# Optimization experiments

Measured on AMD Instinct MI355X. Metric: run time of the kernel, lower is better.

The kernel has to match this reference:

```python
import jax, jax.numpy as jnp
import numpy as np

WS, WS2, UP = 8, 16, 2
DIM, HEADS = 192, 6
HD = DIM // HEADS
SCALE = HD ** -0.5
EPS = 1e-5

def _rel_index():
    r1, c1 = np.meshgrid(np.arange(WS), np.arange(WS), indexing='ij')
    r2, c2 = np.meshgrid(np.arange(WS2), np.arange(WS2), indexing='ij')
    r1, c1 = r1.ravel(), c1.ravel()          # 64 query positions
    r2, c2 = r2.ravel(), c2.ravel()          # 256 kv positions
    rel_row = r1[:, None] - r2[None, :]
    rel_col = c1[:, None] - c2[None, :]
    off = WS * UP - 1    # 15
    span = WS + WS * UP - 1  # 23
    return jnp.asarray((rel_row + off) * span + (rel_col + off))  # (64, 256)

REL_IDX = _rel_index()

def layer_norm(x, w, b):
    m = x.mean(-1, keepdims=True)
    v = ((x - m) ** 2).mean(-1, keepdims=True)
    return (x - m) * jax.lax.rsqrt(v + EPS) * w + b

def window_partition(x, ws):
    B, H, W, C = x.shape
    x = x.reshape(B, H // ws, ws, W // ws, ws, C).transpose(0, 1, 3, 2, 4, 5)
    return x.reshape(-1, ws * ws, C)

def window_reverse(w, ws, H, W, B):
    x = w.reshape(B, H // ws, W // ws, ws, ws, -1).transpose(0, 1, 3, 2, 4, 5)
    return x.reshape(B, H, W, -1)

def setup_inputs() -> dict:
    key = jax.random.key(0)
    ks = jax.random.split(key, 8)
    B, H, W, H2, W2 = 4, 128, 128, 256, 256
    s = 0.02
    return {
        'x': jax.random.normal(ks[0], (B, H * W, DIM), jnp.float32),
        'x2': jax.random.normal(ks[1], (B, H2 * W2, DIM), jnp.float32),
        'norm1_w': jnp.ones((DIM,), jnp.float32),
        'norm1_b': jnp.zeros((DIM,), jnp.float32),
        'qkv_w': jax.random.normal(ks[2], (DIM, DIM), jnp.float32) * s,
        'qkv_b': jnp.zeros((DIM,), jnp.float32),
        'qkv2_w': jax.random.normal(ks[3], (2 * DIM, DIM), jnp.float32) * s,
        'qkv2_b': jnp.zeros((2 * DIM,), jnp.float32),
        'rel_bias': jax.random.normal(ks[4], (23 * 23, HEADS), jnp.float32) * s,
        'proj_w': jax.random.normal(ks[5], (DIM, DIM), jnp.float32) * s,
        'proj_b': jnp.zeros((DIM,), jnp.float32),
        'norm2_w': jnp.ones((DIM,), jnp.float32),
        'norm2_b': jnp.zeros((DIM,), jnp.float32),
        'fc1_w': jax.random.normal(ks[6], (4 * DIM, DIM), jnp.float32) * s,
        'fc1_b': jnp.zeros((4 * DIM,), jnp.float32),
        'fc2_w': jax.random.normal(ks[7], (DIM, 4 * DIM), jnp.float32) * s,
        'fc2_b': jnp.zeros((DIM,), jnp.float32),
        'H': 128, 'W': 128, 'H2': 256, 'W2': 256,
    }

def reference(x, x2, norm1_w, norm1_b, qkv_w, qkv_b, qkv2_w, qkv2_b, rel_bias,
              proj_w, proj_b, norm2_w, norm2_b, fc1_w, fc1_b, fc2_w, fc2_b,
              H, W, H2, W2):
    B, L, C = x.shape
    shortcut = x
    xn = layer_norm(x, norm1_w, norm1_b).reshape(B, H, W, C)
    x2r = x2.reshape(B, H2, W2, C)

    xw = window_partition(xn, WS)      # (nW, 64, C)
    x2w = window_partition(x2r, WS2)   # (nW, 256, C)

    q = (xw @ qkv_w.T + qkv_b).reshape(-1, WS * WS, HEADS, HD).transpose(0, 2, 1, 3)
    kv = (x2w @ qkv2_w.T + qkv2_b).reshape(-1, WS2 * WS2, 2, HEADS, HD).transpose(2, 0, 3, 1, 4)
    k, v = kv[0], kv[1]                # (nW, h, 256, d)

    attn = jnp.einsum('whnd,whmd->whnm', q * SCALE, k)   # (nW, h, 64, 256)
    bias = rel_bias[REL_IDX]                             # (64, 256, h)
    attn = attn + bias.transpose(2, 0, 1)[None]
    attn = jax.nn.softmax(attn, axis=-1)
    out = jnp.einsum('whnm,whmd->wnhd', attn, v).reshape(-1, WS * WS, C)
    out = out @ proj_w.T + proj_b

    x = shortcut + window_reverse(out, WS, H, W, B).reshape(B, H * W, C)
    h = layer_norm(x, norm2_w, norm2_b)
    h = jax.nn.gelu(h @ fc1_w.T + fc1_b, approximate=False)
    x = x + (h @ fc2_w.T + fc2_b)
    return x
```

## Files before the change

### kernel.cpp

```cpp
#include <hip/hip_runtime.h>
#include <hip/hip_bf16.h>
#include <math.h>

typedef unsigned int u32;
typedef unsigned short u16;

typedef __attribute__((ext_vector_type(8))) short bf16x8;
typedef __attribute__((ext_vector_type(4))) float f32x4;

__device__ __forceinline__ float bflo(u32 u){ union{u32 i; float f;} c; c.i = u << 16; return c.f; }
__device__ __forceinline__ float bfhi(u32 u){ union{u32 i; float f;} c; c.i = u & 0xffff0000u; return c.f; }
__device__ __forceinline__ float bfs(u16 s){ union{u32 i; float f;} c; c.i = ((u32)s) << 16; return c.f; }
__device__ __forceinline__ u32 packbf(float a, float b){
  union{float f; u32 i;} ca, cb; ca.f = a; cb.f = b;
  u32 ua = (ca.i + 0x7fffu + ((ca.i >> 16) & 1u)) >> 16;
  u32 ub = (cb.i + 0x7fffu + ((cb.i >> 16) & 1u)) >> 16;
  return (ua & 0xffffu) | (ub << 16);
}
__device__ __forceinline__ u16 bf1(float a){
  union{float f; u32 i;} c; c.f = a;
  return (u16)((c.i + 0x7fffu + ((c.i >> 16) & 1u)) >> 16);
}
__device__ __forceinline__ bf16x8 pack8(float f0,float f1,float f2,float f3,
                                        float f4,float f5,float f6,float f7){
  union { u32 u[4]; bf16x8 v; } cv;
  cv.u[0]=packbf(f0,f1); cv.u[1]=packbf(f2,f3); cv.u[2]=packbf(f4,f5); cv.u[3]=packbf(f6,f7);
  return cv.v;
}
__device__ __forceinline__ float gelu_exact(float v){ return 0.5f*v*(1.0f + erff(v*0.70710678118654752f)); }
__device__ __forceinline__ bool detect_f32(const u32* rawn1){ return (rawn1[0] & 0xFFFFu) == 0u; }

#define SCALE_Q 0.17677669529663687f

#define P_N1W 0
#define P_N1B 192
#define P_N2W 384
#define P_N2B 576
#define P_QKVB 768
#define P_QKV2B 960
#define P_PROJB 1344
#define P_FC1B 1536
#define P_FC2B 2304
#define P_RELB 2496
#define P_TOTAL 5670
#define W_QKV 0
#define W_QKV2 18432
#define W_PROJ 55296
#define W_FC1 73728
#define W_FC2 147456
#define W_TOTAL 221184

__device__ __forceinline__ void stage_w64x192(const u32* __restrict__ src, u32* lds, int tid){
  #pragma unroll
  for (int t = 0; t < 6; ++t) {
    int idx = tid + t*256;
    int j = idx / 24, seg = idx % 24;
    uint4 v = *(const uint4*)(src + (size_t)j*96 + seg*4);
    int byt = (j*384 + seg*16) ^ ((j&7)<<4);
    *(uint4*)((char*)lds + byt) = v;
  }
}
__device__ __forceinline__ bf16x8 lds_w64(const u32* lds, int j, int kt, int g){
  int byt = (j*384 + kt*64 + g*16) ^ ((j&7)<<4);
  return *(const bf16x8*)((const char*)lds + byt);
}
__device__ __forceinline__ bf16x8 lds_w192(const u32* lds, int j, int kk, int g){
  int byt = (j*128 + kk*64 + g*16) ^ ((j&7)<<4);
  return *(const bf16x8*)((const char*)lds + byt);
}

typedef __attribute__((address_space(1))) const u32 gas_u32c;
typedef __attribute__((address_space(3))) u32 las_u32;
__device__ __forceinline__ void gld_lds16(const u32* g, u32* l){
  gas_u32c* gp = (gas_u32c*)(unsigned long long)(size_t)g;
  las_u32*  lp = (las_u32*)(unsigned int)(size_t)l;
  __builtin_amdgcn_global_load_lds(gp, lp, 16, 0, 0);
}
__device__ __forceinline__ void issue_w64x192(const u32* src, u32* lds, int w, int l){
  #pragma unroll
  for (int t = 0; t < 3; ++t) {
    int seg = w + t*8;
    int a = seg*1024 + l*16;
    int j = a / 384;
    int off = a - j*384;
    const u32* g = src + (size_t)j*96 + ((off ^ ((j&7)<<4)) >> 2);
    gld_lds16(g, lds + seg*256);
  }
}
__device__ __forceinline__ void issue_w192x64(const u32* src, int ch, u32* lds, int w, int l){
  #pragma unroll
  for (int t = 0; t < 3; ++t) {
    int seg = w + t*8;
    int a = seg*1024 + l*16;
    int j = a >> 7;
    int off = a & 127;
    const u32* g = src + (size_t)j*384 + ch*32 + ((off ^ ((j&7)<<4)) >> 2);
    gld_lds16(g, lds + seg*256);
  }
}

__global__ __launch_bounds__(256) void k_canon_w(
    const void* qkvw, const void* qkv2w, const void* projw,
    const void* fc1w, const void* fc2w, const u32* rawn1, u32* cw)
{
  int idx = blockIdx.x*256 + threadIdx.x;
  bool isf32 = detect_f32(rawn1);
  const void* src; int off;
  if      (idx < W_QKV2){ src=qkvw;  off=idx; }
  else if (idx < W_PROJ){ src=qkv2w; off=idx-W_QKV2; }
  else if (idx < W_FC1) { src=projw; off=idx-W_PROJ; }
  else if (idx < W_FC2) { src=fc1w;  off=idx-W_FC1; }
  else                  { src=fc2w;  off=idx-W_FC2; }
  u32 o;
  if (isf32) { float2 v = ((const float2*)src)[off]; o = packbf(v.x, v.y); }
  else       { o = ((const u32*)src)[off]; }
  cw[idx] = o;
}

__global__ __launch_bounds__(256) void k_canon_v(
    const void* n1w, const void* n1b, const void* n2w, const void* n2b,
    const void* qkvb, const void* qkv2b, const void* projb,
    const void* fc1b, const void* fc2b, const void* relb,
    const u32* rawn1, float* par)
{
  int idx = blockIdx.x*256 + threadIdx.x;
  if (idx >= P_TOTAL) return;
  bool isf32 = detect_f32(rawn1);
  const void* src; int off;
  if      (idx < P_N1B)  { src=n1w;  off=idx; }
  else if (idx < P_N2W)  { src=n1b;  off=idx-P_N1B; }
  else if (idx < P_N2B)  { src=n2w;  off=idx-P_N2W; }
  else if (idx < P_QKVB) { src=n2b;  off=idx-P_N2B; }
  else if (idx < P_QKV2B){ src=qkvb; off=idx-P_QKVB; }
  else if (idx < P_PROJB){ src=qkv2b;off=idx-P_QKV2B; }
  else if (idx < P_FC1B) { src=projb;off=idx-P_PROJB; }
  else if (idx < P_FC2B) { src=fc1b; off=idx-P_FC1B; }
  else if (idx < P_RELB) { src=fc2b; off=idx-P_FC2B; }
  else                   { src=relb; off=idx-P_RELB; }
  par[idx] = isf32 ? ((const float*)src)[off] : bfs(((const u16*)src)[off]);
}

__global__ __launch_bounds__(256) void k_bias(
    const float* __restrict__ par, float* __restrict__ tbl)
{
  int idx = blockIdx.x*256 + threadIdx.x;
  int h  = idx >> 12;
  int remi = idx & 4095;
  int kt = remi >> 8;
  int qt = (remi >> 6) & 3;
  int ll = idx & 63;
  int lr = ll & 15, g = ll >> 4;
  int q = qt*16 + lr;
  int r1 = q >> 3, c1 = q & 7;
  float vv[4];
  #pragma unroll
  for (int i = 0; i < 4; ++i) {
    int kv = kt*16 + 4*g + i;
    int r2 = kv >> 4, c2 = kv & 15;
    vv[i] = par[P_RELB + ((r1-r2+15)*23 + (c1-c2+15))*6 + h];
  }
  ((float4*)tbl)[idx] = make_float4(vv[0], vv[1], vv[2], vv[3]);
}

__global__ __launch_bounds__(256) void k_qproj(
    const void* __restrict__ x, const u32* __restrict__ rawn1,
    const u32* __restrict__ cw, const float* __restrict__ par,
    u16* __restrict__ q_ws)
{
  __shared__ u32 wbuf[6144];
  int tid = threadIdx.x;
  int l = tid & 63, w = tid >> 6, lr = l & 15, g = l >> 4;
  int wi = blockIdx.x;
  int b = wi >> 8, rem = wi & 255, wh = rem >> 4, ww = rem & 15;
  bool isf32 = detect_f32(rawn1);

  bf16x8 a[6];
  {
    int t = w*16 + lr;
    int r = t >> 3, c = t & 7;
    size_t grow = (size_t)b*16384 + (size_t)(wh*8+r)*128 + (ww*8+c);
    float4 xf[12];
    if (isf32) {
      const float* xp = (const float*)x + grow*192;
      #pragma unroll
      for (int kt = 0; kt < 6; ++kt) {
        xf[kt*2]   = *(const float4*)(xp + kt*32 + 8*g);
        xf[kt*2+1] = *(const float4*)(xp + kt*32 + 8*g + 4);
      }
    } else {
      const u32* xp = (const u32*)x + grow*96;
      #pragma unroll
      for (int kt = 0; kt < 6; ++kt) {
        uint4 u = *(const uint4*)(xp + kt*16 + 4*g);
        xf[kt*2]   = make_float4(bflo(u.x), bfhi(u.x), bflo(u.y), bfhi(u.y));
        xf[kt*2+1] = make_float4(bflo(u.z), bfhi(u.z), bflo(u.w), bfhi(u.w));
      }
    }
    float s = 0.f, s2 = 0.f;
    #pragma unroll
    for (int q8 = 0; q8 < 12; ++q8) {
      s  += xf[q8].x + xf[q8].y + xf[q8].z + xf[q8].w;
      s2 += xf[q8].x*xf[q8].x + xf[q8].y*xf[q8].y + xf[q8].z*xf[q8].z + xf[q8].w*xf[q8].w;
    }
    s += __shfl_xor(s, 16); s2 += __shfl_xor(s2, 16);
    s += __shfl_xor(s, 32); s2 += __shfl_xor(s2, 32);
    float m = s * (1.f/192.f);
    float rstd = rsqrtf(s2*(1.f/192.f) - m*m + 1e-5f);
    #pragma unroll
    for (int kt = 0; kt < 6; ++kt) {
      int k0 = kt*32 + 8*g;
      float4 w0 = *(const float4*)(par + P_N1W + k0);
      float4 w1 = *(const float4*)(par + P_N1W + k0 + 4);
      float4 b0 = *(const float4*)(par + P_N1B + k0);
      float4 b1 = *(const float4*)(par + P_N1B + k0 + 4);
      float4 f0 = xf[kt*2], f1 = xf[kt*2+1];
      a[kt] = pack8((f0.x-m)*rstd*w0.x + b0.x, (f0.y-m)*rstd*w0.y + b0.y,
                    (f0.z-m)*rstd*w0.z + b0.z, (f0.w-m)*rstd*w0.w + b0.w,
                    (f1.x-m)*rstd*w1.x + b1.x, (f1.y-m)*rstd*w1.y + b1.y,
                    (f1.z-m)*rstd*w1.z + b1.z, (f1.w-m)*rstd*w1.w + b1.w);
    }
  }

  for (int ch = 0; ch < 3; ++ch) {
    __syncthreads();
    stage_w64x192(cw + W_QKV + (size_t)(ch*64)*96, wbuf, tid);
    __syncthreads();
    #pragma unroll
    for (int nt2 = 0; nt2 < 4; ++nt2) {
      int j = ch*64 + nt2*16 + lr;
      f32x4 acc = {0.f,0.f,0.f,0.f};
      #pragma unroll
      for (int kt = 0; kt < 6; ++kt) {
        bf16x8 bb = lds_w64(wbuf, nt2*16 + lr, kt, g);
        acc = __builtin_amdgcn_mfma_f32_16x16x32_bf16(a[kt], bb, acc, 0, 0, 0);
      }
      float bj = par[P_QKVB + j];
      int h = j >> 5, d = j & 31;
      #pragma unroll
      for (int i = 0; i < 4; ++i) {
        int n = w*16 + 4*g + i;
        q_ws[(size_t)(wi*6+h)*2048 + (size_t)n*32 + d] = bf1((acc[i] + bj) * SCALE_Q);
      }
    }
  }
}

__global__ __launch_bounds__(256) void k_kvproj(
    const void* __restrict__ x2, const u32* __restrict__ rawn1,
    const u32* __restrict__ cw, const float* __restrict__ par,
    u16* __restrict__ k_ws, u16* __restrict__ v_ws, int win0)
{
  __shared__ u32 wbuf[6144];
  __shared__ u16 otile[64][72];
  int tid = threadIdx.x;
  int l = tid & 63, w = tid >> 6, lr = l & 15, g = l >> 4;
  int lwi = blockIdx.x >> 2, sub = blockIdx.x & 3;
  int wi = win0 + lwi;
  int b = wi >> 8, rem = wi & 255, wh = rem >> 4, ww = rem & 15;
  bool isf32 = detect_f32(rawn1);

  bf16x8 a[6];
  {
    int tt = sub*64 + w*16 + lr;
    int r = tt >> 4, c = tt & 15;
    size_t grow = (size_t)b*65536 + (size_t)(wh*16+r)*256 + (ww*16+c);
    if (isf32) {
      const float4* xp = (const float4*)x2 + grow*48;
      #pragma unroll
      for (int kt = 0; kt < 6; ++kt) {
        float4 f0 = xp[kt*8 + g*2];
        float4 f1 = xp[kt*8 + g*2 + 1];
        a[kt] = pack8(f0.x,f0.y,f0.z,f0.w, f1.x,f1.y,f1.z,f1.w);
      }
    } else {
      const u32* xp = (const u32*)x2 + grow*96;
      #pragma unroll
      for (int kt = 0; kt < 6; ++kt)
        a[kt] = *(const bf16x8*)(xp + kt*16 + g*4);
    }
  }

  for (int ch = 0; ch < 6; ++ch) {
    __syncthreads();
    stage_w64x192(cw + W_QKV2 + (size_t)(ch*64)*96, wbuf, tid);
    __syncthreads();
    if (ch < 3) {
      #pragma unroll
      for (int nt2 = 0; nt2 < 4; ++nt2) {
        int j = ch*64 + nt2*16 + lr;
        f32x4 acc = {0.f,0.f,0.f,0.f};
        #pragma unroll
        for (int kt = 0; kt < 6; ++kt) {
          bf16x8 bb = lds_w64(wbuf, nt2*16 + lr, kt, g);
          acc = __builtin_amdgcn_mfma_f32_16x16x32_bf16(a[kt], bb, acc, 0, 0, 0);
        }
        float bj = par[P_QKV2B + j];
        #pragma unroll
        for (int i = 0; i < 4; ++i)
          otile[w*16 + 4*g + i][nt2*16 + lr] = bf1(acc[i] + bj);
      }
    } else {
      #pragma unroll
      for (int nt2 = 0; nt2 < 4; ++nt2) {
        f32x4 acc = {0.f,0.f,0.f,0.f};
        #pragma unroll
        for (int kt = 0; kt < 6; ++kt) {
          bf16x8 bb = lds_w64(wbuf, nt2*16 + lr, kt, g);
          acc = __builtin_amdgcn_mfma_f32_16x16x32_bf16(bb, a[kt], acc, 0, 0, 0);
        }
        int jl0 = nt2*16 + 4*g;
        int jr0 = (ch-3)*64 + jl0;
        #pragma unroll
        for (int i = 0; i < 4; ++i)
          otile[jl0 + i][w*16 + lr] = bf1(acc[i] + par[P_QKV2B + 192 + jr0 + i]);
      }
    }
    __syncthreads();
    if (ch < 3) {
      #pragma unroll
      for (int t = 0; t < 2; ++t) {
        int u = tid + t*256;
        int hh2 = u >> 8, remu = u & 255;
        int tok = remu >> 2, dseg = remu & 3;
        uint4 v = *(const uint4*)&otile[tok][hh2*32 + dseg*8];
        *(uint4*)(k_ws + (size_t)(lwi*6 + ch*2 + hh2)*8192
                        + (size_t)(sub*64 + tok)*32 + dseg*8) = v;
      }
    } else {
      int nv = ch - 3;
      #pragma unroll
      for (int t = 0; t < 2; ++t) {
        int u = tid + t*256;
        int jrow = u >> 3, seg = u & 7;
        int h = nv*2 + (jrow >> 5), dd = jrow & 31;
        uint4 v = *(const uint4*)&otile[jrow][seg*8];
        *(uint4*)(v_ws + (size_t)(lwi*6 + h)*8192 + (size_t)dd*256
                        + sub*64 + seg*8) = v;
      }
    }
  }
}

__global__ __launch_bounds__(256) void k_attn(
    const u16* __restrict__ q_ws, const u16* __restrict__ k_ws,
    const u16* __restrict__ v_ws, const float* __restrict__ tbl,
    u16* __restrict__ O_ws, int win0)
{
  __shared__ u32 Psh[4*1024];
  __shared__ float msh[2][2][4];
  int tid = threadIdx.x;
  int w = tid >> 6, l = tid & 63;
  int lr = l & 15, g = l >> 4;
  int pairi = w >> 1, half = w & 1;
  int task = blockIdx.x*2 + pairi;
  int lwi = task / 6, h = task - lwi*6;
  int wi = win0 + lwi;

  bf16x8 qb[4];
  {
    const u16* qp = q_ws + (size_t)(wi*6+h)*2048;
    #pragma unroll
    for (int qt = 0; qt < 4; ++qt)
      qb[qt] = *(const bf16x8*)(qp + (qt*16 + lr)*32 + 8*g);
  }
  const u16* kp = k_ws + (size_t)(lwi*6+h)*8192;
  const u16* vp = v_ws + (size_t)(lwi*6+h)*8192;
  const float4* tb4 = (const float4*)tbl + (size_t)h*4096 + l;

  f32x4 ao[2][4];
  #pragma unroll
  for (int dt = 0; dt < 2; ++dt)
    #pragma unroll
    for (int qt = 0; qt < 4; ++qt) ao[dt][qt] = (f32x4){0.f,0.f,0.f,0.f};
  float mreg[4] = {-3.0e38f,-3.0e38f,-3.0e38f,-3.0e38f};
  float sreg[4] = {0.f,0.f,0.f,0.f};
  u32* pbu = Psh + w*1024;

  for (int ch = half*4; ch < half*4 + 4; ++ch) {
    bf16x8 ka0 = *(const bf16x8*)(kp + (2*ch)*512   + lr*32 + 8*g);
    bf16x8 ka1 = *(const bf16x8*)(kp + (2*ch+1)*512 + lr*32 + 8*g);
    f32x4 s0[4], s1[4];
    #pragma unroll
    for (int qt = 0; qt < 4; ++qt) {
      float4 b0 = tb4[(2*ch)*256   + qt*64];
      float4 b1 = tb4[(2*ch+1)*256 + qt*64];
      f32x4 c0; c0[0]=b0.x; c0[1]=b0.y; c0[2]=b0.z; c0[3]=b0.w;
      f32x4 c1; c1[0]=b1.x; c1[1]=b1.y; c1[2]=b1.z; c1[3]=b1.w;
      s0[qt] = __builtin_amdgcn_mfma_f32_16x16x32_bf16(ka0, qb[qt], c0, 0, 0, 0);
      s1[qt] = __builtin_amdgcn_mfma_f32_16x16x32_bf16(ka1, qb[qt], c1, 0, 0, 0);
    }
    #pragma unroll
    for (int qt = 0; qt < 4; ++qt) {
      float pm = fmaxf(fmaxf(fmaxf(s0[qt][0],s0[qt][1]), fmaxf(s0[qt][2],s0[qt][3])),
                       fmaxf(fmaxf(s1[qt][0],s1[qt][1]), fmaxf(s1[qt][2],s1[qt][3])));
      pm = fmaxf(pm, __shfl_xor(pm, 16));
      pm = fmaxf(pm, __shfl_xor(pm, 32));
      if (!__all(pm - mreg[qt] <= 8.0f)) {
        float nm = fmaxf(mreg[qt], pm);
        float resc = __expf(mreg[qt] - nm);
        mreg[qt] = nm;
        sreg[qt] *= resc;
        #pragma unroll
        for (int dt = 0; dt < 2; ++dt) {
          ao[dt][qt][0] *= resc; ao[dt][qt][1] *= resc;
          ao[dt][qt][2] *= resc; ao[dt][qt][3] *= resc;
        }
      }
      float nm = mreg[qt];
      float p00 = __expf(s0[qt][0]-nm), p01 = __expf(s0[qt][1]-nm),
            p02 = __expf(s0[qt][2]-nm), p03 = __expf(s0[qt][3]-nm);
      float p10 = __expf(s1[qt][0]-nm), p11 = __expf(s1[qt][1]-nm),
            p12 = __expf(s1[qt][2]-nm), p13 = __expf(s1[qt][3]-nm);
      float ps = ((p00+p01)+(p02+p03)) + ((p10+p11)+(p12+p13));
      ps += __shfl_xor(ps, 16);
      ps += __shfl_xor(ps, 32);
      sreg[qt] += ps;
      int row = qt*16 + lr;
      int sw = (row & 3) << 2;
      *(uint2*)&pbu[row*16 + ((2*g) ^ sw)]     = make_uint2(packbf(p00,p01), packbf(p02,p03));
      *(uint2*)&pbu[row*16 + ((8 + 2*g) ^ sw)] = make_uint2(packbf(p10,p11), packbf(p12,p13));
    }
    asm volatile("" ::: "memory");
    bf16x8 va0 = *(const bf16x8*)(vp + lr*256        + ch*32 + 8*g);
    bf16x8 va1 = *(const bf16x8*)(vp + (16 + lr)*256 + ch*32 + 8*g);
    #pragma unroll
    for (int qt = 0; qt < 4; ++qt) {
      int row = qt*16 + lr;
      int sw = (row & 3) << 2;
      bf16x8 pa = *(const bf16x8*)&pbu[row*16 + ((4*g) ^ sw)];
      ao[0][qt] = __builtin_amdgcn_mfma_f32_16x16x32_bf16(va0, pa, ao[0][qt], 0, 0, 0);
      ao[1][qt] = __builtin_amdgcn_mfma_f32_16x16x32_bf16(va1, pa, ao[1][qt], 0, 0, 0);
    }
    asm volatile("" ::: "memory");
  }

  __syncthreads();
  if (half == 1) {
    float* dst = (float*)(Psh + pairi*2048);
    #pragma unroll
    for (int dt = 0; dt < 2; ++dt)
      #pragma unroll
      for (int qt = 0; qt < 4; ++qt)
        #pragma unroll
        for (int i = 0; i < 4; ++i)
          dst[(dt*16 + qt*4 + i)*64 + l] = ao[dt][qt][i];
    if (l == 0) {
      msh[pairi][0][0] = mreg[0]; msh[pairi][0][1] = mreg[1];
      msh[pairi][0][2] = mreg[2]; msh[pairi][0][3] = mreg[3];
      msh[pairi][1][0] = sreg[0]; msh[pairi][1][1] = sreg[1];
      msh[pairi][1][2] = sreg[2]; msh[pairi][1][3] = sreg[3];
    }
  }
  __syncthreads();
  if (half == 0) {
    const float* src = (const float*)(Psh + pairi*2048);
    #pragma unroll
    for (int qt = 0; qt < 4; ++qt) {
      float m1 = msh[pairi][0][qt], s1 = msh[pairi][1][qt];
      float M = fmaxf(mreg[qt], m1);
      float e0 = __expf(mreg[qt] - M), e1 = __expf(m1 - M);
      float rs = 1.0f / (sreg[qt]*e0 + s1*e1);
      u16* orow = O_ws + ((size_t)(wi*64) + qt*16 + lr)*192 + h*32;
      #pragma unroll
      for (int dt = 0; dt < 2; ++dt)
        #pragma unroll
        for (int i = 0; i < 4; ++i) {
          float o = ao[dt][qt][i]*e0 + src[(dt*16 + qt*4 + i)*64 + l]*e1;
          orow[dt*16 + 4*g + i] = bf1(o * rs);
        }
    }
  }
}

__global__ __launch_bounds__(256) void k_proj(
    const u16* __restrict__ O_ws, const u32* __restrict__ cw,
    const float* __restrict__ par, const void* __restrict__ x,
    const u32* __restrict__ rawn1, float* __restrict__ xres)
{
  __shared__ u32 wbuf[6144];
  int wi = blockIdx.x;
  int b = wi >> 8, rem = wi & 255, wh = rem >> 4, ww = rem & 15;
  int tid = threadIdx.x;
  int l = tid & 63, w = tid >> 6, lr = l & 15, g = l >> 4;
  bool isf32 = detect_f32(rawn1);
  int t = w*16 + lr;
  const u16* op = O_ws + (size_t)(wi*64 + t)*192;
  bf16x8 a[6];
  #pragma unroll
  for (int kt = 0; kt < 6; ++kt) a[kt] = *(const bf16x8*)(op + kt*32 + 8*g);

  for (int ch = 0; ch < 3; ++ch) {
    __syncthreads();
    stage_w64x192(cw + W_PROJ + (size_t)(ch*64)*96, wbuf, tid);
    __syncthreads();
    #pragma unroll
    for (int nt2 = 0; nt2 < 4; ++nt2) {
      int j = ch*64 + nt2*16 + lr;
      f32x4 acc = {0.f,0.f,0.f,0.f};
      #pragma unroll
      for (int kt = 0; kt < 6; ++kt) {
        bf16x8 bb = lds_w64(wbuf, nt2*16 + lr, kt, g);
        acc = __builtin_amdgcn_mfma_f32_16x16x32_bf16(a[kt], bb, acc, 0, 0, 0);
      }
      float bj = par[P_PROJB + j];
      #pragma unroll
      for (int i = 0; i < 4; ++i) {
        int tok = w*16 + 4*g + i;
        int rr = tok >> 3, cc = tok & 7;
        size_t grow = (size_t)b*16384 + (size_t)(wh*8+rr)*128 + (ww*8+cc);
        float sres = isf32 ? ((const float*)x)[grow*192 + j]
                           : bfs(((const u16*)x)[grow*192 + j]);
        xres[grow*192 + j] = sres + acc[i] + bj;
      }
    }
  }
}

__global__ __launch_bounds__(512) void k_mlp(
    const float* __restrict__ xres, const u32* __restrict__ cw,
    const float* __restrict__ par, float* __restrict__ out)
{
  __shared__ u32 wbufA[6144];
  __shared__ u32 wbufB[6144];
  __shared__ u16 Hc[8][32][64];
  int tid = threadIdx.x;
  int l = tid & 63, w = tid >> 6;
  int lr = l & 15, g = l >> 4;
  size_t row0 = (size_t)blockIdx.x * 256;

  bf16x8 a[2][6];
  #pragma unroll
  for (int mt = 0; mt < 2; ++mt) {
    size_t t = row0 + w*32 + mt*16 + lr;
    const float* xr = xres + t*192;
    float4 xf[12];
    #pragma unroll
    for (int kt = 0; kt < 6; ++kt) {
      xf[kt*2]   = *(const float4*)(xr + kt*32 + 8*g);
      xf[kt*2+1] = *(const float4*)(xr + kt*32 + 8*g + 4);
    }
    float s = 0.f, s2 = 0.f;
    #pragma unroll
    for (int q = 0; q < 12; ++q) {
      s  += xf[q].x + xf[q].y + xf[q].z + xf[q].w;
      s2 += xf[q].x*xf[q].x + xf[q].y*xf[q].y + xf[q].z*xf[q].z + xf[q].w*xf[q].w;
    }
    s += __shfl_xor(s, 16); s2 += __shfl_xor(s2, 16);
    s += __shfl_xor(s, 32); s2 += __shfl_xor(s2, 32);
    float m = s * (1.f/192.f);
    float rstd = rsqrtf(s2*(1.f/192.f) - m*m + 1e-5f);
    #pragma unroll
    for (int kt = 0; kt < 6; ++kt) {
      int k0 = kt*32 + 8*g;
      float4 w0 = *(const float4*)(par + P_N2W + k0);
      float4 w1 = *(const float4*)(par + P_N2W + k0 + 4);
      float4 b0 = *(const float4*)(par + P_N2B + k0);
      float4 b1 = *(const float4*)(par + P_N2B + k0 + 4);
      float4 f0 = xf[kt*2], f1 = xf[kt*2+1];
      a[mt][kt] = pack8((f0.x-m)*rstd*w0.x + b0.x, (f0.y-m)*rstd*w0.y + b0.y,
                        (f0.z-m)*rstd*w0.z + b0.z, (f0.w-m)*rstd*w0.w + b0.w,
                        (f1.x-m)*rstd*w1.x + b1.x, (f1.y-m)*rstd*w1.y + b1.y,
                        (f1.z-m)*rstd*w1.z + b1.z, (f1.w-m)*rstd*w1.w + b1.w);
    }
  }

  f32x4 acc2[2][12];
  #pragma unroll
  for (int mt = 0; mt < 2; ++mt)
    #pragma unroll
    for (int i = 0; i < 12; ++i) acc2[mt][i] = (f32x4){0.f,0.f,0.f,0.f};

  char* hbase = (char*)&Hc[w][0][0];
  const u32* w1p = cw + W_FC1;
  const u32* w2p = cw + W_FC2;

  issue_w64x192(w1p, wbufA, w, l);
  __syncthreads();

  for (int ch = 0; ch < 12; ++ch) {
    issue_w192x64(w2p, ch, wbufB, w, l);
    #pragma unroll
    for (int nt2 = 0; nt2 < 4; ++nt2) {
      f32x4 acc0 = {0.f,0.f,0.f,0.f}, acc1 = {0.f,0.f,0.f,0.f};
      #pragma unroll
      for (int kt = 0; kt < 6; ++kt) {
        bf16x8 bb = lds_w64(wbufA, nt2*16 + lr, kt, g);
        acc0 = __builtin_amdgcn_mfma_f32_16x16x32_bf16(a[0][kt], bb, acc0, 0, 0, 0);
        acc1 = __builtin_amdgcn_mfma_f32_16x16x32_bf16(a[1][kt], bb, acc1, 0, 0, 0);
      }
      float bj = par[P_FC1B + ch*64 + nt2*16 + lr];
      #pragma unroll
      for (int mt = 0; mt < 2; ++mt) {
        f32x4 acc = mt ? acc1 : acc0;
        #pragma unroll
        for (int i = 0; i < 4; ++i) {
          int row = mt*16 + 4*g + i;
          int byt = (row*128 + (nt2*16+lr)*2) ^ ((row&7)<<4);
          *(u16*)(hbase + byt) = bf1(gelu_exact(acc[i] + bj));
        }
      }
    }
    __syncthreads();
    if (ch < 11) issue_w64x192(w1p + (size_t)((ch+1)*64)*96, wbufA, w, l);
    #pragma unroll
    for (int kk = 0; kk < 2; ++kk) {
      bf16x8 a20, a21;
      {
        int row0h = lr, row1h = 16 + lr;
        a20 = *(const bf16x8*)(hbase + ((row0h*128 + kk*64 + g*16) ^ ((row0h&7)<<4)));
        a21 = *(const bf16x8*)(hbase + ((row1h*128 + kk*64 + g*16) ^ ((row1h&7)<<4)));
      }
      #pragma unroll
      for (int nt = 0; nt < 12; ++nt) {
        bf16x8 bb = lds_w192(wbufB, nt*16 + lr, kk, g);
        acc2[0][nt] = __builtin_amdgcn_mfma_f32_16x16x32_bf16(a20, bb, acc2[0][nt], 0, 0, 0);
        acc2[1][nt] = __builtin_amdgcn_mfma_f32_16x16x32_bf16(a21, bb, acc2[1][nt], 0, 0, 0);
      }
    }
    __syncthreads();
  }

  #pragma unroll
  for (int mt = 0; mt < 2; ++mt) {
    size_t trow = row0 + w*32 + mt*16 + 4*g;
    #pragma unroll
    for (int nt = 0; nt < 12; ++nt) {
      int j = nt*16 + lr;
      float bj = par[P_FC2B + j];
      #pragma unroll
      for (int i = 0; i < 4; ++i)
        out[(trow+i)*192 + j] = xres[(trow+i)*192 + j] + acc2[mt][nt][i] + bj;
    }
  }
}

extern "C" void kernel_launch(void* const* d_in, const int* in_sizes, int n_in,
                              void* d_out, int out_size, void* d_ws, size_t ws_size,
                              hipStream_t stream) {
  const void* x      = d_in[0];
  const void* x2     = d_in[1];
  const void* n1w    = d_in[2];
  const void* n1b    = d_in[3];
  const void* qkv_w  = d_in[4];
  const void* qkv_b  = d_in[5];
  const void* qkv2_w = d_in[6];
  const void* qkv2_b = d_in[7];
  const void* relb   = d_in[8];
  const void* proj_w = d_in[9];
  const void* proj_b = d_in[10];
  const void* n2w    = d_in[11];
  const void* n2b    = d_in[12];
  const void* fc1_w  = d_in[13];
  const void* fc1_b  = d_in[14];
  const void* fc2_w  = d_in[15];
  const void* fc2_b  = d_in[16];
  const u32* rawn1   = (const u32*)d_in[2];
  float* out = (float*)d_out;

  int nslice = (ws_size >= 303290520ull) ? 1 : (ws_size >= 202700000ull) ? 2 : 4;
  int nw = 1024 / nslice;
  size_t kvb = (size_t)nw * 98304;

  char* ws = (char*)d_ws;
  u16*   q_ws = (u16*)ws;
  u16*   k_ws = (u16*)(ws + 25165824);
  u16*   v_ws = (u16*)(ws + 25165824 + kvb);
  u16*   O_ws = (u16*)(ws + 25165824 + 2*kvb);
  float* xres = (float*)(ws + 50331648 + 2*kvb);
  u32*   cw   = (u32*)(ws + 100663296 + 2*kvb);
  float* tbl  = (float*)(ws + 100663296 + 2*kvb + 884736);
  float* par  = (float*)(ws + 100663296 + 2*kvb + 884736 + 393216);

  k_canon_w<<<W_TOTAL/256, 256, 0, stream>>>(qkv_w, qkv2_w, proj_w, fc1_w, fc2_w, rawn1, cw);
  k_canon_v<<<(P_TOTAL+255)/256, 256, 0, stream>>>(n1w, n1b, n2w, n2b, qkv_b, qkv2_b,
                                                   proj_b, fc1_b, fc2_b, relb, rawn1, par);
  k_bias  <<<96, 256, 0, stream>>>(par, tbl);
  k_qproj <<<1024, 256, 0, stream>>>(x, rawn1, cw, par, q_ws);
  for (int s = 0; s < nslice; ++s) {
    int win0 = s*nw;
    k_kvproj<<<nw*4, 256, 0, stream>>>(x2, rawn1, cw, par, k_ws, v_ws, win0);
    k_attn  <<<nw*3, 256, 0, stream>>>(q_ws, k_ws, v_ws, tbl, O_ws, win0);
  }
  k_proj  <<<1024, 256, 0, stream>>>(O_ws, cw, par, x, rawn1, xres);
  k_mlp   <<< 256, 512, 0, stream>>>(xres, cw, par, out);
}
```

Measured before the change: 634.1 us.

## Double-buffer KV-projection weight chunks with async global-to-LDS prefetch

The KV projection kernel now processes the 384 output channels in twelve 32-row chunks instead of six 64-row chunks. Each next chunk's weights are prefetched into an alternate LDS buffer with global_load_lds while the current chunk runs its MFMAs, replacing the old synchronous stage-then-sync pattern. This aims to hide weight-load latency behind compute. In exchange there are twice as many loop iterations and barriers, and smaller per-chunk work.

Result: no change. 630.8 us (-0.5%).

```diff
diff --git a/kernel.cpp b/kernel.cpp
--- a/kernel.cpp
+++ b/kernel.cpp
@@ -87,6 +87,17 @@
     gld_lds16(g, lds + seg*256);
   }
 }
+__device__ __forceinline__ void issue_w32x192_t256(const u32* src, u32* lds, int w, int l){
+  #pragma unroll
+  for (int t = 0; t < 3; ++t) {
+    int seg = w + t*4;
+    int a = seg*1024 + l*16;
+    int j = a / 384;
+    int off = a - j*384;
+    const u32* g = src + (size_t)j*96 + ((off ^ ((j&7)<<4)) >> 2);
+    gld_lds16(g, lds + seg*256);
+  }
+}
 __device__ __forceinline__ void issue_w192x64(const u32* src, int ch, u32* lds, int w, int l){
   #pragma unroll
   for (int t = 0; t < 3; ++t) {
@@ -250,7 +261,8 @@
     const u32* __restrict__ cw, const float* __restrict__ par,
     u16* __restrict__ k_ws, u16* __restrict__ v_ws, int win0)
 {
-  __shared__ u32 wbuf[6144];
+  __shared__ u32 wbufA[3072];
+  __shared__ u32 wbufB[3072];
   __shared__ u16 otile[64][72];
   int tid = threadIdx.x;
   int l = tid & 63, w = tid >> 6, lr = l & 15, g = l >> 4;
@@ -259,6 +271,8 @@
   int b = wi >> 8, rem = wi & 255, wh = rem >> 4, ww = rem & 15;
   bool isf32 = detect_f32(rawn1);
 
+  issue_w32x192_t256(cw + W_QKV2, wbufA, w, l);
+
   bf16x8 a[6];
   {
     int tt = sub*64 + w*16 + lr;
@@ -279,65 +293,59 @@
         a[kt] = *(const bf16x8*)(xp + kt*16 + g*4);
     }
   }
-
-  for (int ch = 0; ch < 6; ++ch) {
-    __syncthreads();
-    stage_w64x192(cw + W_QKV2 + (size_t)(ch*64)*96, wbuf, tid);
-    __syncthreads();
-    if (ch < 3) {
-      #pragma unroll
-      for (int nt2 = 0; nt2 < 4; ++nt2) {
-        int j = ch*64 + nt2*16 + lr;
+  __syncthreads();
+
+  for (int c = 0; c < 12; ++c) {
+    const u32* buf = (c & 1) ? wbufB : wbufA;
+    u32* nxt = (c & 1) ? wbufA : wbufB;
+    if (c < 11)
+      issue_w32x192_t256(cw + W_QKV2 + (size_t)((c+1)*32)*96, nxt, w, l);
+    if (c < 6) {
+      #pragma unroll
+      for (int nt2 = 0; nt2 < 2; ++nt2) {
+        int jl = nt2*16 + lr;
         f32x4 acc = {0.f,0.f,0.f,0.f};
         #pragma unroll
         for (int kt = 0; kt < 6; ++kt) {
-          bf16x8 bb = lds_w64(wbuf, nt2*16 + lr, kt, g);
+          bf16x8 bb = lds_w64(buf, jl, kt, g);
           acc = __builtin_amdgcn_mfma_f32_16x16x32_bf16(a[kt], bb, acc, 0, 0, 0);
         }
-        float bj = par[P_QKV2B + j];
+        float bj = par[P_QKV2B + c*32 + jl];
         #pragma unroll
         for (int i = 0; i < 4; ++i)
-          otile[w*16 + 4*g + i][nt2*16 + lr] = bf1(acc[i] + bj);
+          otile[w*16 + 4*g + i][jl] = bf1(acc[i] + bj);
+      }
+      __syncthreads();
+      {
+        int tok = tid >> 2, dseg = tid & 3;
+        uint4 v = *(const uint4*)&otile[tok][dseg*8];
+        *(uint4*)(k_ws + (size_t)(lwi*6 + c)*8192
+                        + (size_t)(sub*64 + tok)*32 + dseg*8) = v;
       }
     } else {
-      #pragma unroll
-      for (int nt2 = 0; nt2 < 4; ++nt2) {
+      int nv = c - 6;
+      #pragma unroll
+      for (int nt2 = 0; nt2 < 2; ++nt2) {
         f32x4 acc = {0.f,0.f,0.f,0.f};
         #pragma unroll
         for (int kt = 0; kt < 6; ++kt) {
-          bf16x8 bb = lds_w64(wbuf, nt2*16 + lr, kt, g);
+          bf16x8 bb = lds_w64(buf, nt2*16 + lr, kt, g);
           acc = __builtin_amdgcn_mfma_f32_16x16x32_bf16(bb, a[kt], acc, 0, 0, 0);
         }
         int jl0 = nt2*16 + 4*g;
-        int jr0 = (ch-3)*64 + jl0;
         #pragma unroll
         for (int i = 0; i < 4; ++i)
-          otile[jl0 + i][w*16 + lr] = bf1(acc[i] + par[P_QKV2B + 192 + jr0 + i]);
+          otile[jl0 + i][w*16 + lr] = bf1(acc[i] + par[P_QKV2B + 192 + nv*32 + jl0 + i]);
+      }
+      __syncthreads();
+      {
+        int jrow = tid >> 3, seg = tid & 7;
+        uint4 v = *(const uint4*)&otile[jrow][seg*8];
+        *(uint4*)(v_ws + (size_t)(lwi*6 + nv)*8192 + (size_t)jrow*256
+                        + sub*64 + seg*8) = v;
       }
     }
     __syncthreads();
-    if (ch < 3) {
-      #pragma unroll
-      for (int t = 0; t < 2; ++t) {
-        int u = tid + t*256;
-        int hh2 = u >> 8, remu = u & 255;
-        int tok = remu >> 2, dseg = remu & 3;
-        uint4 v = *(const uint4*)&otile[tok][hh2*32 + dseg*8];
-        *(uint4*)(k_ws + (size_t)(lwi*6 + ch*2 + hh2)*8192
-                        + (size_t)(sub*64 + tok)*32 + dseg*8) = v;
-      }
-    } else {
-      int nv = ch - 3;
-      #pragma unroll
-      for (int t = 0; t < 2; ++t) {
-        int u = tid + t*256;
-        int jrow = u >> 3, seg = u & 7;
-        int h = nv*2 + (jrow >> 5), dd = jrow & 31;
-        uint4 v = *(const uint4*)&otile[jrow][seg*8];
-        *(uint4*)(v_ws + (size_t)(lwi*6 + h)*8192 + (size_t)dd*256
-                        + sub*64 + seg*8) = v;
-      }
-    }
   }
 }
 
```
